# Optimization experiments

Measured on AMD Instinct MI355X. Metric: run time of the kernel, lower is better.

Reference implementation:

```python
import jax, jax.numpy as jnp
import numpy as np

ALPHA = 0.9        # synaptic decay (hidden layers; layer 0 uses 0*syn + h)
BETA = 0.85        # membrane leak
THRESHOLD = 1.0
SIM_TIME = 50
SCALE = 100.0      # SurrGradSpike.scale


@jax.custom_vjp
def spike_fn(x):
    # Heaviside step: 1.0 where x > 0 (strict, matching torch `input > 0`)
    return (x > 0).astype(x.dtype)

def _spike_fwd(x):
    return spike_fn(x), x

def _spike_bwd(x, g):
    # normalized fast-sigmoid surrogate gradient (Zenke & Ganguli 2018)
    return (g / (SCALE * jnp.abs(x) + 1.0) ** 2,)

spike_fn.defvjp(_spike_fwd, _spike_bwd)


def setup_inputs() -> dict:
    key = jax.random.key(0)
    k0, k1, k2, k3 = jax.random.split(key, 4)
    return {
        "inputs": jax.random.normal(k0, (128, 1024), dtype=jnp.float32),
        "W0": jax.random.normal(k1, (1024, 2048), dtype=jnp.float32),
        "W1": jax.random.normal(k2, (2048, 2048), dtype=jnp.float32),
        "W2": jax.random.normal(k3, (2048, 512), dtype=jnp.float32),
    }


def _dsnn_forward(inputs, weights):
    batch = inputs.shape[0]
    n_layers = len(weights)
    syn0 = tuple(jnp.zeros((batch, W.shape[1]), dtype=inputs.dtype) for W in weights)
    mem0 = tuple(jnp.zeros((batch, W.shape[1]), dtype=inputs.dtype) for W in weights)

    def step(carry, _):
        syn, mem = carry
        new_syn, new_mem = [], []
        prev_spk = None
        for l, W in enumerate(weights):
            # feedforward drive: static input at layer 0, current-step spikes after
            h = inputs @ W if l == 0 else prev_spk @ W
            # layer 0: new_syn = 0*syn + h ; others: alpha*syn + h
            s = h if l == 0 else ALPHA * syn[l] + h
            m = BETA * mem[l] + s
            mthr = m - THRESHOLD
            out = spike_fn(mthr)
            if l < n_layers - 1:
                # hard reset to 0 where spiked (output layer never resets)
                m = jnp.where(mthr > 0, jnp.zeros_like(m), m)
            prev_spk = out
            new_syn.append(s)
            new_mem.append(m)
        return (tuple(new_syn), tuple(new_mem)), None

    (syn, mem), _ = jax.lax.scan(step, (syn0, mem0), None, length=SIM_TIME)
    # torch returns mem_rec[-1][-1]: output-layer membrane at final timestep
    return mem[-1]


def reference(inputs, W0, W1, W2):
    return _dsnn_forward(inputs, (W0, W1, W2))
```

## Files before the change

### kernel.cpp

```cpp
#include <hip/hip_runtime.h>
#include <hip/hip_bf16.h>

#define ALPHA 0.9f
#define BETA  0.85f
#define TSIM  50
#define BATCH 128
#define N0    1024
#define N1    2048
#define N2    2048
#define N3    512

#define A50   0.00515379f
#define B50   0.000295764f
#define INVAB 20.0f

typedef __attribute__((ext_vector_type(8))) short bf16x8;
typedef __attribute__((ext_vector_type(8))) unsigned short ushort8;
typedef __attribute__((ext_vector_type(4))) float f32x4;

#define GLOBAL_AS __attribute__((address_space(1)))
#define LDS_AS    __attribute__((address_space(3)))

#define R32(X) X(0) X(1) X(2) X(3) X(4) X(5) X(6) X(7) X(8) X(9) X(10) X(11) \
               X(12) X(13) X(14) X(15) X(16) X(17) X(18) X(19) X(20) X(21)   \
               X(22) X(23) X(24) X(25) X(26) X(27) X(28) X(29) X(30) X(31)
#define R18(X) X(32) X(33) X(34) X(35) X(36) X(37) X(38) X(39) X(40) X(41)   \
               X(42) X(43) X(44) X(45) X(46) X(47) X(48) X(49)
#define R50(X) R32(X) R18(X)

#define DECLC(t)   float c##t = 0.f;
#define PROBELO(t) c##t += w * (float)((lo >> (t)) & 1u);
#define PROBEHI(t) c##t += w * (float)((hi >> ((t) - 32)) & 1u);
#define PROBE4LO(t) c##t += w0 * (float)((lo0 >> (t)) & 1u); \
                    c##t += w1 * (float)((lo1 >> (t)) & 1u); \
                    c##t += w2 * (float)((lo2 >> (t)) & 1u); \
                    c##t += w3 * (float)((lo3 >> (t)) & 1u);
#define PROBE4HI(t) c##t += w0 * (float)((hi0 >> ((t) - 32)) & 1u); \
                    c##t += w1 * (float)((hi1 >> ((t) - 32)) & 1u); \
                    c##t += w2 * (float)((hi2 >> ((t) - 32)) & 1u); \
                    c##t += w3 * (float)((hi3 >> ((t) - 32)) & 1u);
#define STEPT(t)                                                  \
    s = ALPHA * s + (base + c##t);                                \
    m = BETA * m + s;                                             \
    if (m - 1.f > 0.f) { a2 += (pa - pb) * INVAB; m = 0.f; }      \
    pa *= inva;                                                   \
    pb *= invb;

__global__ __launch_bounds__(256) void gemm_f32_splitk(const float* __restrict__ A,
                                                       const float* __restrict__ B,
                                                       float* __restrict__ Cp,
                                                       int M, int N, int K, int KC) {
    __shared__ float As[16][65];
    __shared__ float Bs[16][68];

    const int tid = threadIdx.x;
    const int tx  = tid % 16;
    const int ty  = tid / 16;
    const int bx  = blockIdx.x;
    const int by  = blockIdx.y;
    const int z   = blockIdx.z;

    float acc[4][4] = {};

    const int ar = tid / 4;
    const int ak = (tid % 4) * 4;
    const int br = tid / 16;
    const int bc = (tid % 16) * 4;

    const int kbeg = z * KC;
    for (int k0 = kbeg; k0 < kbeg + KC; k0 += 16) {
        float4 av = *(const float4*)&A[(size_t)(by * 64 + ar) * K + k0 + ak];
        As[ak + 0][ar] = av.x;
        As[ak + 1][ar] = av.y;
        As[ak + 2][ar] = av.z;
        As[ak + 3][ar] = av.w;
        float4 bv = *(const float4*)&B[(size_t)(k0 + br) * N + bx * 64 + bc];
        *(float4*)&Bs[br][bc] = bv;
        __syncthreads();

#pragma unroll
        for (int kk = 0; kk < 16; ++kk) {
            float a0 = As[kk][ty * 4 + 0];
            float a1 = As[kk][ty * 4 + 1];
            float a2 = As[kk][ty * 4 + 2];
            float a3 = As[kk][ty * 4 + 3];
            float b0 = Bs[kk][tx * 4 + 0];
            float b1 = Bs[kk][tx * 4 + 1];
            float b2 = Bs[kk][tx * 4 + 2];
            float b3 = Bs[kk][tx * 4 + 3];
            acc[0][0] += a0 * b0; acc[0][1] += a0 * b1; acc[0][2] += a0 * b2; acc[0][3] += a0 * b3;
            acc[1][0] += a1 * b0; acc[1][1] += a1 * b1; acc[1][2] += a1 * b2; acc[1][3] += a1 * b3;
            acc[2][0] += a2 * b0; acc[2][1] += a2 * b1; acc[2][2] += a2 * b2; acc[2][3] += a2 * b3;
            acc[3][0] += a3 * b0; acc[3][1] += a3 * b1; acc[3][2] += a3 * b2; acc[3][3] += a3 * b3;
        }
        __syncthreads();
    }

#pragma unroll
    for (int i = 0; i < 4; ++i) {
        float4 v = make_float4(acc[i][0], acc[i][1], acc[i][2], acc[i][3]);
        *(float4*)&Cp[((size_t)z * M + by * 64 + ty * 4 + i) * N + bx * 64 + tx * 4] = v;
    }
}

__global__ __launch_bounds__(256) void scan_l0_classify(const float* __restrict__ P0,
                                                        __hip_bfloat16* __restrict__ C0,
                                                        int* __restrict__ jlist0,
                                                        unsigned long long* __restrict__ mask0,
                                                        int* __restrict__ count0) {
    const int b     = blockIdx.x;
    const int chunk = blockIdx.y;
    const int tid   = threadIdx.x;
    const int j     = chunk * 256 + tid;
    const int lane  = tid & 63;
    const int wv    = tid >> 6;

    float h = 0.f;
#pragma unroll
    for (int z = 0; z < 8; ++z) h += P0[((size_t)z * BATCH + b) * N1 + j];

    float m = 0.f;
    unsigned long long mask = 0ull;
#pragma unroll
    for (int t = 0; t < TSIM; ++t) {
        m = BETA * m + h;
        if (m - 1.f > 0.f) { mask |= (1ull << t); m = 0.f; }
    }
    const unsigned long long FULL = (1ull << TSIM) - 1ull;
    C0[(size_t)b * N1 + j] = __float2bfloat16((mask == FULL) ? 1.f : 0.f);

    const bool has = (mask != 0ull) && (mask != FULL);
    const unsigned long long bal = __ballot(has);

    __shared__ int wcnt[4];
    if (lane == 0) wcnt[wv] = __popcll(bal);
    __syncthreads();
    int base = 0;
#pragma unroll
    for (int w = 0; w < 4; ++w)
        if (w < wv) base += wcnt[w];
    const int pos = base + __popcll(bal & ((1ull << lane) - 1ull));

    const size_t lbase = (size_t)(b * 8 + chunk) * 256;
    if (has) {
        jlist0[lbase + pos] = j;
        mask0[lbase + pos]  = mask;
    }
    if (tid == 0) count0[b * 8 + chunk] = wcnt[0] + wcnt[1] + wcnt[2] + wcnt[3];
}

__global__ __launch_bounds__(256) void gemm3_bn64_fused(const __hip_bfloat16* __restrict__ A,
                                                        const float* __restrict__ W,
                                                        float* __restrict__ Cp, int KC) {
    __shared__ alignas(16) __hip_bfloat16 As[128 * 32];
    __shared__ alignas(16) __hip_bfloat16 Bhs[64 * 32];
    __shared__ alignas(16) __hip_bfloat16 Bls[64 * 32];

    constexpr int BK = 32;
    const int M = BATCH, N = N2, K = N1;

    const int tid  = threadIdx.x;
    const int wave = tid >> 6;
    const int lane = tid & 63;
    const int quad = lane >> 4;
    const int l16  = lane & 15;

    const int n0 = blockIdx.x * 64;
    const int z  = blockIdx.y;
    const int wm = wave * 32;

    f32x4 acc[2][4] = {};

    const __hip_bfloat16* agp[2];
    int aoff[2];
#pragma unroll
    for (int i = 0; i < 2; ++i) {
        const int c = i * 256 + tid;
        agp[i]  = A + (size_t)(c >> 2) * K + (c & 3) * 8;
        aoff[i] = c * 8;
    }

    const int bn  = tid >> 2;
    const int bkb = (tid & 3) * 8;

    const int kbeg = z * KC;
    for (int k0 = kbeg; k0 < kbeg + KC; k0 += BK) {
#pragma unroll
        for (int i = 0; i < 2; ++i)
            __builtin_amdgcn_global_load_lds((const GLOBAL_AS void*)(agp[i] + k0),
                                             (LDS_AS void*)&As[aoff[i]], 16, 0, 0);

        float wv[8];
#pragma unroll
        for (int u = 0; u < 8; ++u)
            wv[u] = W[(size_t)(k0 + bkb + u) * N + n0 + bn];

        ushort8 vh, vl;
#pragma unroll
        for (int u = 0; u < 8; ++u) {
            const float w = wv[u];
            const __hip_bfloat16 hi = __float2bfloat16(w);
            const float lo = w - __bfloat162float(hi);
            const __hip_bfloat16 lb = __float2bfloat16(lo);
            vh[u] = *(const unsigned short*)&hi;
            vl[u] = *(const unsigned short*)&lb;
        }
        *(ushort8*)&Bhs[bn * BK + bkb] = vh;
        *(ushort8*)&Bls[bn * BK + bkb] = vl;
        __syncthreads();

        bf16x8 af[2], bhf[4], blf[4];
#pragma unroll
        for (int i = 0; i < 2; ++i)
            af[i] = *(const bf16x8*)&As[(wm + i * 16 + l16) * BK + quad * 8];
#pragma unroll
        for (int j = 0; j < 4; ++j) {
            bhf[j] = *(const bf16x8*)&Bhs[(j * 16 + l16) * BK + quad * 8];
            blf[j] = *(const bf16x8*)&Bls[(j * 16 + l16) * BK + quad * 8];
        }
#pragma unroll
        for (int i = 0; i < 2; ++i)
#pragma unroll
            for (int j = 0; j < 4; ++j) {
                acc[i][j] = __builtin_amdgcn_mfma_f32_16x16x32_bf16(af[i], bhf[j], acc[i][j], 0, 0, 0);
                acc[i][j] = __builtin_amdgcn_mfma_f32_16x16x32_bf16(af[i], blf[j], acc[i][j], 0, 0, 0);
            }
        __syncthreads();
    }

#pragma unroll
    for (int i = 0; i < 2; ++i)
#pragma unroll
        for (int j = 0; j < 4; ++j)
#pragma unroll
            for (int r = 0; r < 4; ++r)
                Cp[((size_t)z * M + wm + i * 16 + quad * 4 + r) * N + n0 + j * 16 + l16] =
                    acc[i][j][r];
}

__global__ __launch_bounds__(256, 2) void h1_scan_a2(const float* __restrict__ PB1,
                                                     const float* __restrict__ W1,
                                                     const int* __restrict__ jlist0,
                                                     const unsigned long long* __restrict__ mask0,
                                                     const int* __restrict__ count0,
                                                     float* __restrict__ A2) {
    const int b  = blockIdx.x;
    const int jc = blockIdx.y * 256 + threadIdx.x;

    float base = 0.f;
#pragma unroll
    for (int z = 0; z < 16; ++z) base += PB1[((size_t)z * BATCH + b) * N2 + jc];

    R50(DECLC)

    for (int c = 0; c < 8; ++c) {
        const int cnt      = count0[b * 8 + c];
        const size_t lbase = (size_t)(b * 8 + c) * 256;
        int e = 0;
        for (; e + 4 <= cnt; e += 4) {
            const int j0 = jlist0[lbase + e + 0];
            const int j1 = jlist0[lbase + e + 1];
            const int j2 = jlist0[lbase + e + 2];
            const int j3 = jlist0[lbase + e + 3];
            const float w0 = W1[(size_t)j0 * N2 + jc];
            const float w1 = W1[(size_t)j1 * N2 + jc];
            const float w2 = W1[(size_t)j2 * N2 + jc];
            const float w3 = W1[(size_t)j3 * N2 + jc];
            const unsigned long long ma = mask0[lbase + e + 0];
            const unsigned long long mb = mask0[lbase + e + 1];
            const unsigned long long mc = mask0[lbase + e + 2];
            const unsigned long long md = mask0[lbase + e + 3];
            const unsigned lo0 = (unsigned)ma, hi0 = (unsigned)(ma >> 32);
            const unsigned lo1 = (unsigned)mb, hi1 = (unsigned)(mb >> 32);
            const unsigned lo2 = (unsigned)mc, hi2 = (unsigned)(mc >> 32);
            const unsigned lo3 = (unsigned)md, hi3 = (unsigned)(md >> 32);
            R32(PROBE4LO)
            R18(PROBE4HI)
        }
        for (; e < cnt; ++e) {
            const unsigned long long mk = mask0[lbase + e];
            const int j                 = jlist0[lbase + e];
            const float w               = W1[(size_t)j * N2 + jc];
            const unsigned lo = (unsigned)mk, hi = (unsigned)(mk >> 32);
            R32(PROBELO)
            R18(PROBEHI)
        }
    }

    float s = 0.f, m = 0.f, a2 = 0.f;
    float pa = A50, pb = B50;
    const float inva = 1.0f / ALPHA, invb = 1.0f / BETA;
    R50(STEPT)

    A2[(size_t)b * N2 + jc] = a2;
}

__global__ __launch_bounds__(256) void reduce_out(const float* __restrict__ PB2,
                                                  float* __restrict__ out) {
    const int idx = blockIdx.x * 256 + threadIdx.x;
    float v = 0.f;
#pragma unroll
    for (int z = 0; z < 16; ++z) v += PB2[(size_t)z * (BATCH * N3) + idx];
    out[idx] = v;
}

extern "C" void kernel_launch(void* const* d_in, const int* in_sizes, int n_in,
                              void* d_out, int out_size, void* d_ws, size_t ws_size,
                              hipStream_t stream) {
    const float* inputs = (const float*)d_in[0];
    const float* W0     = (const float*)d_in[1];
    const float* W1     = (const float*)d_in[2];
    const float* W2     = (const float*)d_in[3];
    float* out = (float*)d_out;

    float* P0  = (float*)d_ws;
    float* PB1 = P0 + 8 * BATCH * N1;
    float* A2  = PB1 + 16 * BATCH * N2;
    float* PB2 = A2 + BATCH * N2;
    unsigned long long* mk0 = (unsigned long long*)(PB2 + 16 * BATCH * N3);
    __hip_bfloat16* C0bf = (__hip_bfloat16*)(mk0 + BATCH * 8 * 256);
    int* jl0  = (int*)(C0bf + (size_t)BATCH * N1);
    int* cnt0 = jl0 + BATCH * 8 * 256;

    gemm_f32_splitk<<<dim3(N1 / 64, BATCH / 64, 8), 256, 0, stream>>>(
        inputs, W0, P0, BATCH, N1, N0, N0 / 8);

    scan_l0_classify<<<dim3(BATCH, N1 / 256), 256, 0, stream>>>(P0, C0bf, jl0, mk0, cnt0);

    gemm3_bn64_fused<<<dim3(N2 / 64, 16), 256, 0, stream>>>(C0bf, W1, PB1, N1 / 16);

    h1_scan_a2<<<dim3(BATCH, N2 / 256), 256, 0, stream>>>(
        PB1, W1, jl0, mk0, cnt0, A2);

    gemm_f32_splitk<<<dim3(N3 / 64, BATCH / 64, 16), 256, 0, stream>>>(
        A2, W2, PB2, BATCH, N3, N2, N2 / 16);

    reduce_out<<<(BATCH * N3) / 256, 256, 0, stream>>>(PB2, out);
}
```

Measured before the change: 137.9 us.

## Run final layer GEMM on bf16 MFMA with split hi/lo precision

```diff
diff --git a/kernel.cpp b/kernel.cpp
--- a/kernel.cpp
+++ b/kernel.cpp
@@ -50,7 +50,7 @@
                                                        const float* __restrict__ B,
                                                        float* __restrict__ Cp,
                                                        int M, int N, int K, int KC) {
-    __shared__ float As[16][65];
+    __shared__ float As[16][68];
     __shared__ float Bs[16][68];
 
     const int tid = threadIdx.x;
@@ -80,14 +80,10 @@
 
 #pragma unroll
         for (int kk = 0; kk < 16; ++kk) {
-            float a0 = As[kk][ty * 4 + 0];
-            float a1 = As[kk][ty * 4 + 1];
-            float a2 = As[kk][ty * 4 + 2];
-            float a3 = As[kk][ty * 4 + 3];
-            float b0 = Bs[kk][tx * 4 + 0];
-            float b1 = Bs[kk][tx * 4 + 1];
-            float b2 = Bs[kk][tx * 4 + 2];
-            float b3 = Bs[kk][tx * 4 + 3];
+            const float4 a  = *(const float4*)&As[kk][ty * 4];
+            const float4 bq = *(const float4*)&Bs[kk][tx * 4];
+            const float a0 = a.x, a1 = a.y, a2 = a.z, a3 = a.w;
+            const float b0 = bq.x, b1 = bq.y, b2 = bq.z, b3 = bq.w;
             acc[0][0] += a0 * b0; acc[0][1] += a0 * b1; acc[0][2] += a0 * b2; acc[0][3] += a0 * b3;
             acc[1][0] += a1 * b0; acc[1][1] += a1 * b1; acc[1][2] += a1 * b2; acc[1][3] += a1 * b3;
             acc[2][0] += a2 * b0; acc[2][1] += a2 * b1; acc[2][2] += a2 * b2; acc[2][3] += a2 * b3;
@@ -235,6 +231,106 @@
 #pragma unroll
             for (int r = 0; r < 4; ++r)
                 Cp[((size_t)z * M + wm + i * 16 + quad * 4 + r) * N + n0 + j * 16 + l16] =
+                    acc[i][j][r];
+}
+
+__global__ __launch_bounds__(256) void gemm2_mfma(const float* __restrict__ A,
+                                                  const float* __restrict__ W,
+                                                  float* __restrict__ Cp, int KC) {
+    __shared__ alignas(16) __hip_bfloat16 Ahs[128 * 32];
+    __shared__ alignas(16) __hip_bfloat16 Als[128 * 32];
+    __shared__ alignas(16) __hip_bfloat16 Bhs[32 * 32];
+    __shared__ alignas(16) __hip_bfloat16 Bls[32 * 32];
+
+    constexpr int BK = 32;
+    const int tid  = threadIdx.x;
+    const int wave = tid >> 6;
+    const int lane = tid & 63;
+    const int quad = lane >> 4;
+    const int l16  = lane & 15;
+
+    const int n0 = blockIdx.x * 32;
+    const int z  = blockIdx.y;
+    const int wm = wave * 32;
+
+    f32x4 acc[2][2] = {};
+
+    const int ar = tid >> 1;
+    const int ao = (tid & 1) * 16;
+    const int bn = tid & 31;
+    const int bq = (tid >> 5) * 4;
+
+    const int kbeg = z * KC;
+    for (int k0 = kbeg; k0 < kbeg + KC; k0 += BK) {
+        float af[16];
+#pragma unroll
+        for (int q = 0; q < 4; ++q) {
+            float4 v = *(const float4*)&A[(size_t)ar * N2 + k0 + ao + q * 4];
+            af[q * 4 + 0] = v.x; af[q * 4 + 1] = v.y;
+            af[q * 4 + 2] = v.z; af[q * 4 + 3] = v.w;
+        }
+#pragma unroll
+        for (int h = 0; h < 2; ++h) {
+            ushort8 vh, vl;
+#pragma unroll
+            for (int u = 0; u < 8; ++u) {
+                const float a = af[h * 8 + u];
+                const __hip_bfloat16 hi = __float2bfloat16(a);
+                const float lo = a - __bfloat162float(hi);
+                const __hip_bfloat16 lb = __float2bfloat16(lo);
+                vh[u] = *(const unsigned short*)&hi;
+                vl[u] = *(const unsigned short*)&lb;
+            }
+            *(ushort8*)&Ahs[ar * BK + ao + h * 8] = vh;
+            *(ushort8*)&Als[ar * BK + ao + h * 8] = vl;
+        }
+
+        {
+            float wf[4];
+#pragma unroll
+            for (int u = 0; u < 4; ++u)
+                wf[u] = W[(size_t)(k0 + bq + u) * N3 + n0 + bn];
+#pragma unroll
+            for (int u = 0; u < 4; ++u) {
+                const float w = wf[u];
+                const __hip_bfloat16 hi = __float2bfloat16(w);
+                const float lo = w - __bfloat162float(hi);
+                const __hip_bfloat16 lb = __float2bfloat16(lo);
+                Bhs[bn * BK + bq + u] = hi;
+                Bls[bn * BK + bq + u] = lb;
+            }
+        }
+        __syncthreads();
+
+        bf16x8 ah[2], al[2], bh[2], bl[2];
+#pragma unroll
+        for (int i = 0; i < 2; ++i) {
+            ah[i] = *(const bf16x8*)&Ahs[(wm + i * 16 + l16) * BK + quad * 8];
+            al[i] = *(const bf16x8*)&Als[(wm + i * 16 + l16) * BK + quad * 8];
+        }
+#pragma unroll
+        for (int j = 0; j < 2; ++j) {
+            bh[j] = *(const bf16x8*)&Bhs[(j * 16 + l16) * BK + quad * 8];
+            bl[j] = *(const bf16x8*)&Bls[(j * 16 + l16) * BK + quad * 8];
+        }
+#pragma unroll
+        for (int i = 0; i < 2; ++i)
+#pragma unroll
+            for (int j = 0; j < 2; ++j) {
+                acc[i][j] = __builtin_amdgcn_mfma_f32_16x16x32_bf16(ah[i], bh[j], acc[i][j], 0, 0, 0);
+                acc[i][j] = __builtin_amdgcn_mfma_f32_16x16x32_bf16(ah[i], bl[j], acc[i][j], 0, 0, 0);
+                acc[i][j] = __builtin_amdgcn_mfma_f32_16x16x32_bf16(al[i], bh[j], acc[i][j], 0, 0, 0);
+            }
+        __syncthreads();
+    }
+
+#pragma unroll
+    for (int i = 0; i < 2; ++i)
+#pragma unroll
+        for (int j = 0; j < 2; ++j)
+#pragma unroll
+            for (int r = 0; r < 4; ++r)
+                Cp[((size_t)z * BATCH + wm + i * 16 + quad * 4 + r) * N3 + n0 + j * 16 + l16] =
                     acc[i][j][r];
 }
 
@@ -332,8 +428,7 @@
     h1_scan_a2<<<dim3(BATCH, N2 / 256), 256, 0, stream>>>(
         PB1, W1, jl0, mk0, cnt0, A2);
 
-    gemm_f32_splitk<<<dim3(N3 / 64, BATCH / 64, 16), 256, 0, stream>>>(
-        A2, W2, PB2, BATCH, N3, N2, N2 / 16);
+    gemm2_mfma<<<dim3(N3 / 32, 16), 256, 0, stream>>>(A2, W2, PB2, N2 / 16);
 
     reduce_out<<<(BATCH * N3) / 256, 256, 0, stream>>>(PB2, out);
 }
```

After: 133.6 us (median of 2 runs). 3.1% less time.
